# Kernel tuning notes

Measured on AMD Instinct MI355X. Metric: run time of the kernel, lower is better.

Reference implementation:

```python
import jax, jax.numpy as jnp
import numpy as np

# dims
P = 512          # perception_vector_size
A_DIM = 64       # action_vector_size
D_MODEL = 256
D_STATE = 16
D_CONV = 4
D_INNER = 2 * D_MODEL      # expand=2 -> 512
DT_RANK = D_MODEL // 16    # ceil(256/16) = 16
BATCH = 8192


def setup_inputs() -> dict:
    key = jax.random.key(0)
    ks = jax.random.split(key, 12)
    s = lambda k, shp, sc=0.02: (jax.random.normal(k, shp, jnp.float32) * sc)
    return {
        "perception": jax.random.normal(ks[0], (BATCH, P), jnp.float32),
        # Brain linears
        "W_in": s(ks[1], (D_MODEL, P)), "b_in": jnp.zeros((D_MODEL,), jnp.float32),
        "mu_w": s(ks[2], (A_DIM, D_MODEL)), "mu_b": jnp.zeros((A_DIM,), jnp.float32),
        "ls_w": s(ks[3], (A_DIM, D_MODEL)), "ls_b": jnp.zeros((A_DIM,), jnp.float32),
        # Mamba params (mamba_ssm Mamba(d_model=256, d_state=16, d_conv=4, expand=2))
        "in_proj_w": s(ks[4], (2 * D_INNER, D_MODEL)),            # no bias
        "conv_w": s(ks[5], (D_INNER, D_CONV), 0.1),               # depthwise causal conv
        "conv_b": jnp.zeros((D_INNER,), jnp.float32),
        "x_proj_w": s(ks[6], (DT_RANK + 2 * D_STATE, D_INNER)),   # no bias
        "dt_proj_w": s(ks[7], (D_INNER, DT_RANK), 0.1),
        "dt_proj_b": s(ks[8], (D_INNER,), 0.1),
        # S4D real init: A_log[d, n] = log(n+1)
        "A_log": jnp.log(jnp.broadcast_to(jnp.arange(1, D_STATE + 1, dtype=jnp.float32), (D_INNER, D_STATE))),
        "Dskip": jnp.ones((D_INNER,), jnp.float32),
        "out_proj_w": s(ks[9], (D_MODEL, D_INNER)),               # no bias
    }


def _mamba(x, in_proj_w, conv_w, conv_b, x_proj_w, dt_proj_w, dt_proj_b, A_log, Dskip):
    # x: [B, L, d_model]
    Bsz, L, _ = x.shape
    xz = x @ in_proj_w.T                       # [B, L, 2*D_INNER]
    u, z = jnp.split(xz, 2, axis=-1)           # each [B, L, D_INNER]
    # causal depthwise conv1d (padding d_conv-1 on the left), then SiLU
    u_pad = jnp.pad(u, ((0, 0), (D_CONV - 1, 0), (0, 0)))
    idx = jnp.arange(L)[:, None] + jnp.arange(D_CONV)[None, :]   # [L, K]
    windows = u_pad[:, idx, :]                 # [B, L, K, D_INNER]
    u = jnp.einsum('blkc,ck->blc', windows, conv_w) + conv_b
    u = jax.nn.silu(u)
    # input-dependent SSM params
    x_dbl = u @ x_proj_w.T                     # [B, L, dt_rank + 2*d_state]
    dt, Bm, Cm = jnp.split(x_dbl, [DT_RANK, DT_RANK + D_STATE], axis=-1)
    delta = jax.nn.softplus(dt @ dt_proj_w.T + dt_proj_b)  # [B, L, D_INNER]
    A = -jnp.exp(A_log)                        # [D_INNER, D_STATE]

    def step(h, inp):
        u_t, dl, b_t, c_t = inp                # [B,D],[B,D],[B,N],[B,N]
        dA = jnp.exp(dl[..., None] * A)        # [B, D, N]
        h = dA * h + dl[..., None] * b_t[:, None, :] * u_t[..., None]
        y = jnp.einsum('bdn,bn->bd', h, c_t)
        return h, y

    h0 = jnp.zeros((Bsz, D_INNER, D_STATE), u.dtype)
    xs = (u.transpose(1, 0, 2), delta.transpose(1, 0, 2),
          Bm.transpose(1, 0, 2), Cm.transpose(1, 0, 2))
    _, ys = jax.lax.scan(step, h0, xs)         # ys: [L, B, D_INNER]
    y = ys.transpose(1, 0, 2) + Dskip * u      # skip connection D*u
    return y * jax.nn.silu(z)


def reference(perception, W_in, b_in, mu_w, mu_b, ls_w, ls_b,
              in_proj_w, conv_w, conv_b, x_proj_w, dt_proj_w, dt_proj_b,
              A_log, Dskip, out_proj_w):
    x = (perception @ W_in.T + b_in)[:, None, :]     # [B, 1, d_model]
    y = _mamba(x, in_proj_w, conv_w, conv_b, x_proj_w,
               dt_proj_w, dt_proj_b, A_log, Dskip)   # [B, 1, D_INNER]
    h = (y @ out_proj_w.T)[:, 0, :]                  # [B, d_model]
    mu = jnp.tanh(h @ mu_w.T + mu_b)
    log_std = jnp.clip(h @ ls_w.T + ls_b, -5.0, 2.0)
    return mu, log_std
```

## Files before the change

### kernel.cpp

```cpp
#include <hip/hip_runtime.h>
#include <hip/hip_fp16.h>
#include <cmath>

#define BATCH 8192

typedef short bf16x8 __attribute__((ext_vector_type(8)));
typedef float f32x4 __attribute__((ext_vector_type(4)));
typedef float f32x16 __attribute__((ext_vector_type(16)));

__device__ __forceinline__ void split2(float x, unsigned short& h, unsigned short& l){
    unsigned u = __float_as_uint(x);
    unsigned hr = u + 0x7fffu + ((u >> 16) & 1u);
    unsigned short hs = (unsigned short)(hr >> 16);
    float hf = __uint_as_float(((unsigned)hs) << 16);
    float d = x - hf;
    unsigned v = __float_as_uint(d);
    unsigned short ls = (unsigned short)((v + 0x7fffu + ((v >> 16) & 1u)) >> 16);
    h = hs; l = ls;
}
__device__ __forceinline__ float fsig(float x){ return 1.f / (1.f + __expf(-x)); }
__device__ __forceinline__ float ftanh(float x){
    x = fminf(fmaxf(x, -10.f), 10.f);
    const float e = __expf(2.f*x);
    return (e - 1.f) / (e + 1.f);
}
__device__ __forceinline__ void async_copy16(void* lds, const void* g){
    __builtin_amdgcn_global_load_lds(
        (const __attribute__((address_space(1))) unsigned int*)g,
        (__attribute__((address_space(3))) unsigned int*)lds, 16, 0, 0);
}


__global__ __launch_bounds__(256) void prep_all(
    const float* __restrict__ percep,
    const float* __restrict__ in_proj, const float* __restrict__ W_in,
    const float* __restrict__ b_in,
    const float* __restrict__ mu_w, const float* __restrict__ ls_w,
    const float* __restrict__ conv_w, const float* __restrict__ conv_b,
    const float* __restrict__ out_proj, const float* __restrict__ x_proj,
    unsigned short* __restrict__ W1h, unsigned short* __restrict__ W1l,
    unsigned short* __restrict__ Wth, unsigned short* __restrict__ Wtl,
    unsigned short* __restrict__ Xph, unsigned short* __restrict__ Xpl,
    unsigned short* __restrict__ Ph, unsigned short* __restrict__ Pl,
    float* __restrict__ b1)
{
    __shared__ float As[16][68];
    __shared__ float Ws[16][68];
    __shared__ unsigned short Lh[4096];
    __shared__ unsigned short Ll[4096];

    const int bx = blockIdx.x, by = blockIdx.y;
    const int tid = threadIdx.x;
    if (bx >= 20){
        const int s = (bx-20)*8 + by;
        const int band = s >> 4, ks = s & 15;
        const size_t tbase = (size_t)s*4096;
#pragma unroll
        for (int g=0; g<2; ++g){
            const int u = g*256 + tid;
            const int row = u >> 2, piece = u & 3;
            const float* src = percep + (size_t)(band*128 + row)*512 + ks*32 + piece*8;
            const float4 v0 = *reinterpret_cast<const float4*>(src);
            const float4 v1 = *reinterpret_cast<const float4*>(src+4);
            unsigned short h[8], l[8];
            split2(v0.x,h[0],l[0]); split2(v0.y,h[1],l[1]);
            split2(v0.z,h[2],l[2]); split2(v0.w,h[3],l[3]);
            split2(v1.x,h[4],l[4]); split2(v1.y,h[5],l[5]);
            split2(v1.z,h[6],l[6]); split2(v1.w,h[7],l[7]);
            uint4 H, L;
            H.x=(unsigned)h[0]|((unsigned)h[1]<<16); H.y=(unsigned)h[2]|((unsigned)h[3]<<16);
            H.z=(unsigned)h[4]|((unsigned)h[5]<<16); H.w=(unsigned)h[6]|((unsigned)h[7]<<16);
            L.x=(unsigned)l[0]|((unsigned)l[1]<<16); L.y=(unsigned)l[2]|((unsigned)l[3]<<16);
            L.z=(unsigned)l[4]|((unsigned)l[5]<<16); L.w=(unsigned)l[6]|((unsigned)l[7]<<16);
            const int off = piece*1024 + row*8;
            *reinterpret_cast<uint4*>(&Lh[off]) = H;
            *reinterpret_cast<uint4*>(&Ll[off]) = L;
        }
        __syncthreads();
#pragma unroll
        for (int g=0; g<2; ++g){
            const int f = g*256 + tid;
            *reinterpret_cast<uint4*>(&Ph[tbase + f*8]) = *reinterpret_cast<const uint4*>(&Lh[f*8]);
            *reinterpret_cast<uint4*>(&Pl[tbase + f*8]) = *reinterpret_cast<const uint4*>(&Ll[f*8]);
        }
        return;
    }
    if (bx == 18){
        const int lane = tid & 63, w = tid >> 6;
        const float4 bv = *reinterpret_cast<const float4*>(&b_in[lane*4]);
        const int nbase = by*128 + w*32;
#pragma unroll 4
        for (int i=0;i<32;i++){
            const int n = nbase + i;
            const float4 av = *reinterpret_cast<const float4*>(&in_proj[(size_t)n*256 + lane*4]);
            float p = av.x*bv.x + av.y*bv.y + av.z*bv.z + av.w*bv.w;
#pragma unroll
            for (int off=32; off; off>>=1) p += __shfl_xor(p, off, 64);
            if (lane == 0)
                b1[n] = (n < 512) ? fmaf(p, conv_w[n*4+3], conv_b[n]) : p;
        }
        return;
    }
    if (bx == 19){
        const int c0 = by*64;
#pragma unroll
        for (int p=0;p<16;p++){
            const int idx = p*256 + tid;
            const int rrow = idx >> 6;
            const int c = c0 + (idx & 63);
            const float v = (rrow < 48) ? x_proj[(size_t)rrow*512 + c] : 0.f;
            unsigned short h,l; split2(v,h,l);
            const int ks = c >> 5, r = (c >> 3) & 3, pos = c & 7;
            const size_t off = (size_t)ks*2048 + (r*64 + rrow)*8 + pos;
            Xph[off]=h; Xpl[off]=l;
        }
        return;
    }
    const float* A; unsigned short *Oh, *Ol; int m0; bool wt;
    const float* B;
    if (bx < 16){ A = in_proj + (size_t)bx*64*256; B = W_in; Oh=W1h; Ol=W1l; m0=bx*64; wt=false; }
    else { A = (bx==16 ? mu_w : ls_w); B = out_proj; Oh=Wth; Ol=Wtl; m0=(bx-16)*64; wt=true; }
    const int n0 = by*64;

    const int tm = tid/16, tn = tid%16;
    float acc[4][4];
#pragma unroll
    for (int i=0;i<4;i++)
#pragma unroll
      for (int j=0;j<4;j++) acc[i][j]=0.f;

    for (int k0=0;k0<256;k0+=16){
        {
            const int kf = tid & 3, mm = tid >> 2;
            float4 v = *reinterpret_cast<const float4*>(A + (size_t)mm*256 + k0 + kf*4);
            As[kf*4+0][mm]=v.x; As[kf*4+1][mm]=v.y; As[kf*4+2][mm]=v.z; As[kf*4+3][mm]=v.w;
        }
        {
            const int nn4 = tid & 15, kk = tid >> 4;
            float4 v = *reinterpret_cast<const float4*>(B + (size_t)(k0+kk)*512 + n0 + nn4*4);
            *reinterpret_cast<float4*>(&Ws[kk][nn4*4]) = v;
        }
        __syncthreads();
#pragma unroll
        for (int k=0;k<16;k++){
            const float4 av = *reinterpret_cast<const float4*>(&As[k][tm*4]);
            const float4 bv = *reinterpret_cast<const float4*>(&Ws[k][tn*4]);
            float a[4]={av.x,av.y,av.z,av.w}, b[4]={bv.x,bv.y,bv.z,bv.w};
#pragma unroll
            for (int i=0;i<4;i++)
#pragma unroll
                for (int j=0;j<4;j++) acc[i][j] = fmaf(a[i], b[j], acc[i][j]);
        }
        __syncthreads();
    }
#pragma unroll
    for (int i=0;i<4;i++){
        const int gm = m0 + tm*4 + i;
        const float s = (!wt && gm < 512) ? conv_w[gm*4+3] : 1.f;
        const int n = n0 + tn*4;
        unsigned short h[4], l[4];
#pragma unroll
        for (int j=0;j<4;j++) split2(acc[i][j]*s, h[j], l[j]);
        const int ks = n >> 5, r = (n >> 3) & 3, pos = n & 7;
        size_t off;
        if (wt) off = (size_t)ks*4096 + (r*128 + gm)*8 + pos;
        else    off = (size_t)((gm>>7)*16 + ks)*4096 + (r*128 + (gm&127))*8 + pos;
        *reinterpret_cast<ushort4*>(&Oh[off]) = make_ushort4(h[0],h[1],h[2],h[3]);
        *reinterpret_cast<ushort4*>(&Ol[off]) = make_ushort4(l[0],l[1],l[2],l[3]);
    }
}

__global__ __launch_bounds__(256,2) void mgemm5(
    const unsigned short* __restrict__ AhT, const unsigned short* __restrict__ AlT,
    const unsigned short* __restrict__ BhT, const unsigned short* __restrict__ BlT,
    const float* __restrict__ bias,
    float* __restrict__ O0, __half* __restrict__ O1)
{
    constexpr int TM=128, TN=128, WM=64, WN=64;
    constexpr int WAVES_N = TN/WN;
    constexpr int MT = WM/32, NT = WN/32;
    constexpr int PL = 4096;
    constexpr int BUF = 4*PL;
    constexpr int NK = 16;
    __shared__ unsigned short sm[2*BUF];

    const int tid = threadIdx.x;
    const int mb = blockIdx.x, nb = blockIdx.y;
    const int m0 = mb * TM, n0 = nb * TN;
    const int lane = tid & 63, wid = tid >> 6;
    const int half = lane >> 5, l32 = lane & 31;
    const int wm = (wid / WAVES_N) * WM;
    const int wn = (wid % WAVES_N) * WN;

    f32x16 acc[MT][NT];
#pragma unroll
    for (int i=0;i<MT;i++)
#pragma unroll
      for (int j=0;j<NT;j++)
#pragma unroll
        for (int r=0;r<16;r++) acc[i][j][r] = 0.f;

    auto dmaAll = [&](int k, int b){
        unsigned short* base = sm + b*BUF;
        const unsigned short* Ah = AhT + (size_t)(mb*16 + k)*PL;
        const unsigned short* Al = AlT + (size_t)(mb*16 + k)*PL;
        const unsigned short* Bh = BhT + (size_t)(nb*16 + k)*PL;
        const unsigned short* Bl = BlT + (size_t)(nb*16 + k)*PL;
#pragma unroll
        for (int it=0; it<2; ++it){
            const int f = it*256 + tid;
            const int wb = (it*256 + wid*64)*8;
            async_copy16(base +        wb, Ah + f*8);
            async_copy16(base +   PL + wb, Al + f*8);
            async_copy16(base + 2*PL + wb, Bh + f*8);
            async_copy16(base + 3*PL + wb, Bl + f*8);
        }
    };

    dmaAll(0, 0);

    for (int k=0; k<NK; ++k){
        const int cur = k & 1, nxt = cur ^ 1;
        __syncthreads();
        if (k+1 < NK) dmaAll(k+1, nxt);

        const unsigned short* bufc = sm + cur*BUF;
        bf16x8 ah[2][MT], al[2][MT], bh[2][NT], bl[2][NT];
#pragma unroll
        for (int j=0;j<2;j++){
            const int r = j*2 + half;
#pragma unroll
            for (int mt=0; mt<MT; ++mt){
                const int off = (r*TM + wm + mt*32 + l32)*8;
                ah[j][mt] = *reinterpret_cast<const bf16x8*>(&bufc[off]);
                al[j][mt] = *reinterpret_cast<const bf16x8*>(&bufc[PL + off]);
            }
#pragma unroll
            for (int nt=0; nt<NT; ++nt){
                const int off = (r*TN + wn + nt*32 + l32)*8;
                bh[j][nt] = *reinterpret_cast<const bf16x8*>(&bufc[2*PL + off]);
                bl[j][nt] = *reinterpret_cast<const bf16x8*>(&bufc[3*PL + off]);
            }
        }
#pragma unroll
        for (int j=0;j<2;j++){
#pragma unroll
            for (int mt=0; mt<MT; ++mt)
#pragma unroll
            for (int nt=0; nt<NT; ++nt)
                acc[mt][nt] = __builtin_amdgcn_mfma_f32_32x32x16_bf16(ah[j][mt], bh[j][nt], acc[mt][nt], 0,0,0);
#pragma unroll
            for (int mt=0; mt<MT; ++mt)
#pragma unroll
            for (int nt=0; nt<NT; ++nt)
                acc[mt][nt] = __builtin_amdgcn_mfma_f32_32x32x16_bf16(al[j][mt], bh[j][nt], acc[mt][nt], 0,0,0);
#pragma unroll
            for (int mt=0; mt<MT; ++mt)
#pragma unroll
            for (int nt=0; nt<NT; ++nt)
                acc[mt][nt] = __builtin_amdgcn_mfma_f32_32x32x16_bf16(ah[j][mt], bl[j][nt], acc[mt][nt], 0,0,0);
        }
    }

#pragma unroll
    for (int mt=0; mt<MT; ++mt)
#pragma unroll
    for (int nt=0; nt<NT; ++nt)
#pragma unroll
    for (int r=0; r<16; ++r){
        const int row = m0 + wm + mt*32 + (r&3) + 8*(r>>2) + 4*half;
        const int col = n0 + wn + nt*32 + l32;
        float v = acc[mt][nt][r] + bias[col];
        if (col < 512) O0[(size_t)row*512 + col] = v * fsig(v);
        else           O1[(size_t)row*512 + (col-512)] = __float2half(v);
    }
}

__global__ __launch_bounds__(256) void tail_fused(
    const float* __restrict__ Uf, const __half* __restrict__ Zh,
    const unsigned short* __restrict__ XphT, const unsigned short* __restrict__ XplT,
    const unsigned short* __restrict__ WthT, const unsigned short* __restrict__ WtlT,
    const float* __restrict__ dtw, const float* __restrict__ dtb,
    const float* __restrict__ dskip,
    const float* __restrict__ mu_b, const float* __restrict__ ls_b,
    float* __restrict__ mu_o, float* __restrict__ ls_o)
{
    constexpr int TM=32, TN=64;
    constexpr int P1_APL = 1024;
    constexpr int P1_BPL = 2048;
    constexpr int P1_BUF = 2*P1_APL + 2*P1_BPL;
    constexpr int PSTR = 264;
    __shared__ unsigned short sW[16384];
    __shared__ unsigned short sYh[16*PSTR];
    __shared__ unsigned short sYl[16*PSTR];
    __shared__ float sxd[32][49];
    __shared__ float sBC[32];

    const int tid = threadIdx.x;
    const int m0 = blockIdx.x * TM;
    const int lane = tid & 63, wid = tid >> 6;
    const int quad = lane >> 4, l16 = lane & 15;
    const int wm = (wid >> 1) * 16;
    const int wn = (wid & 1) * 32;

    f32x4 acc[2];
    acc[0] = (f32x4){0.f,0.f,0.f,0.f};
    acc[1] = (f32x4){0.f,0.f,0.f,0.f};

    float4 areg[2];
    const int am = tid & 31, ar = (tid >> 5) & 3;

    auto loadA = [&](int k){
        if (tid < 128){
            const float* src = Uf + (size_t)(m0+am)*512 + k*32 + ar*8;
            areg[0] = *reinterpret_cast<const float4*>(src);
            areg[1] = *reinterpret_cast<const float4*>(src+4);
        }
    };
    auto dmaB = [&](int k, int b){
        unsigned short* dst = sW + b*P1_BUF + 2*P1_APL;
        const int wb = wid*64*8;
        async_copy16(dst + wb,          XphT + (size_t)k*P1_BPL + tid*8);
        async_copy16(dst + P1_BPL + wb, XplT + (size_t)k*P1_BPL + tid*8);
    };
    auto writeA = [&](int b){
        if (tid < 128){
            unsigned short* dh = sW + b*P1_BUF;
            unsigned short* dl = dh + P1_APL;
            const float* p = reinterpret_cast<const float*>(&areg[0]);
            unsigned short h[8], l[8];
#pragma unroll
            for (int j=0;j<8;j++) split2(p[j], h[j], l[j]);
            uint4 H, L;
            H.x=(unsigned)h[0]|((unsigned)h[1]<<16); H.y=(unsigned)h[2]|((unsigned)h[3]<<16);
            H.z=(unsigned)h[4]|((unsigned)h[5]<<16); H.w=(unsigned)h[6]|((unsigned)h[7]<<16);
            L.x=(unsigned)l[0]|((unsigned)l[1]<<16); L.y=(unsigned)l[2]|((unsigned)l[3]<<16);
            L.z=(unsigned)l[4]|((unsigned)l[5]<<16); L.w=(unsigned)l[6]|((unsigned)l[7]<<16);
            const int f = (tid >> 5)*32 + am;
            *reinterpret_cast<uint4*>(&dh[f*8]) = H;
            *reinterpret_cast<uint4*>(&dl[f*8]) = L;
        }
    };

    loadA(0); dmaB(0,0); writeA(0);
    for (int k=0; k<16; ++k){
        const int cur = k & 1, nxt = cur ^ 1;
        __syncthreads();
        const bool pf = (k+1 < 16);
        if (pf){ loadA(k+1); dmaB(k+1, nxt); }
        const unsigned short* bufc = sW + cur*P1_BUF;
        bf16x8 ah, al2, bh[2], bl[2];
        {
            const int off = (quad*TM + wm + l16)*8;
            ah  = *reinterpret_cast<const bf16x8*>(&bufc[off]);
            al2 = *reinterpret_cast<const bf16x8*>(&bufc[P1_APL + off]);
        }
#pragma unroll
        for (int nt=0; nt<2; ++nt){
            const int off = (quad*TN + wn + nt*16 + l16)*8;
            bh[nt] = *reinterpret_cast<const bf16x8*>(&bufc[2*P1_APL + off]);
            bl[nt] = *reinterpret_cast<const bf16x8*>(&bufc[2*P1_APL + P1_BPL + off]);
        }
#pragma unroll
        for (int nt=0; nt<2; ++nt)
            acc[nt] = __builtin_amdgcn_mfma_f32_16x16x32_bf16(ah, bh[nt], acc[nt], 0,0,0);
#pragma unroll
        for (int nt=0; nt<2; ++nt)
            acc[nt] = __builtin_amdgcn_mfma_f32_16x16x32_bf16(al2, bh[nt], acc[nt], 0,0,0);
#pragma unroll
        for (int nt=0; nt<2; ++nt)
            acc[nt] = __builtin_amdgcn_mfma_f32_16x16x32_bf16(ah, bl[nt], acc[nt], 0,0,0);
        if (pf) writeA(nxt);
    }

#pragma unroll
    for (int nt=0; nt<2; ++nt)
#pragma unroll
    for (int r=0; r<4; ++r){
        const int row = wm + quad*4 + r;
        const int col = wn + nt*16 + l16;
        if (col < 48) sxd[row][col] = acc[nt][r];
    }
    __syncthreads();
    if (tid < 32){
        float bc = 0.f;
#pragma unroll
        for (int n=0;n<16;n++) bc = fmaf(sxd[tid][16+n], sxd[tid][32+n], bc);
        sBC[tid] = bc;
    }
    __syncthreads();

    const int wm2 = (wid >> 1) * 16;
    const int wn2 = (wid & 1) * 64;
    f32x4 oacc[4];
#pragma unroll
    for (int j=0;j<4;j++) oacc[j] = (f32x4){0.f,0.f,0.f,0.f};

    const int q = tid >> 6, dd = tid & 63;

    auto dmaW = [&](int ks, int b){
        unsigned short* dst = sW + b*8192;
#pragma unroll
        for (int it=0; it<2; ++it){
            const int f = it*256 + tid;
            const int wb = (it*256 + wid*64)*8;
            async_copy16(dst + wb,        WthT + (size_t)ks*4096 + f*8);
            async_copy16(dst + 4096 + wb, WtlT + (size_t)ks*4096 + f*8);
        }
    };

    for (int c=0; c<4; ++c){
        const int c0 = c*128;
        const int d0 = c0 + 2*dd, d1 = d0 + 1;
        float w0[16], w1[16];
#pragma unroll
        for (int j=0;j<4;j++){
            float4 a = *reinterpret_cast<const float4*>(&dtw[d0*16 + j*4]);
            w0[j*4]=a.x; w0[j*4+1]=a.y; w0[j*4+2]=a.z; w0[j*4+3]=a.w;
            float4 b = *reinterpret_cast<const float4*>(&dtw[d1*16 + j*4]);
            w1[j*4]=b.x; w1[j*4+1]=b.y; w1[j*4+2]=b.z; w1[j*4+3]=b.w;
        }
        const float db0 = dtb[d0], db1 = dtb[d1];
        const float dk0 = dskip[d0], dk1 = dskip[d1];

        __syncthreads();
        const int lk = 2*dd;
        const unsigned yidx = (unsigned)((lk>>3)*PSTR + (lk&7)) >> 1;
#pragma unroll 2
        for (int rr=0; rr<8; ++rr){
            const int r = q*8 + rr;
            float xr[16];
#pragma unroll
            for (int j=0;j<16;j++) xr[j] = sxd[r][j];
            const float bc = sBC[r];
            float t0 = db0, t1 = db1;
#pragma unroll
            for (int j=0;j<16;j++){ t0 = fmaf(xr[j], w0[j], t0); t1 = fmaf(xr[j], w1[j], t1); }
            const float dl0 = (t0 > 20.f) ? t0 : __logf(1.f + __expf(t0));
            const float dl1 = (t1 > 20.f) ? t1 : __logf(1.f + __expf(t1));
            const size_t off = (size_t)(m0+r)*512;
            const float2 uv = *reinterpret_cast<const float2*>(&Uf[off + d0]);
            const __half2 zv = *reinterpret_cast<const __half2*>(&Zh[off + d0]);
            const float z0 = __low2float(zv), z1 = __high2float(zv);
            const float y0 = uv.x * fmaf(dl0, bc, dk0) * (z0 * fsig(z0));
            const float y1 = uv.y * fmaf(dl1, bc, dk1) * (z1 * fsig(z1));
            unsigned short h0,l0,h1,l1;
            split2(y0,h0,l0); split2(y1,h1,l1);
            const unsigned idx = yidx + (unsigned)(r*4);
            reinterpret_cast<unsigned*>(sYh)[idx] = (unsigned)h0 | ((unsigned)h1<<16);
            reinterpret_cast<unsigned*>(sYl)[idx] = (unsigned)l0 | ((unsigned)l1<<16);
        }
        dmaW(c*4, 0);
        for (int s=0; s<4; ++s){
            __syncthreads();
            if (s < 3) dmaW(c*4 + s+1, (s+1)&1);
            const unsigned short* bw = sW + (s&1)*8192;
            bf16x8 ya, yl2, bh2[4], bl2[4];
            {
                const int aoff = (4*s + quad)*PSTR + (wm2 + l16)*8;
                ya  = *reinterpret_cast<const bf16x8*>(&sYh[aoff]);
                yl2 = *reinterpret_cast<const bf16x8*>(&sYl[aoff]);
            }
#pragma unroll
            for (int nt=0; nt<4; ++nt){
                const int boff = (quad*128 + wn2 + nt*16 + l16)*8;
                bh2[nt] = *reinterpret_cast<const bf16x8*>(&bw[boff]);
                bl2[nt] = *reinterpret_cast<const bf16x8*>(&bw[4096 + boff]);
            }
#pragma unroll
            for (int nt=0; nt<4; ++nt)
                oacc[nt] = __builtin_amdgcn_mfma_f32_16x16x32_bf16(ya, bh2[nt], oacc[nt], 0,0,0);
#pragma unroll
            for (int nt=0; nt<4; ++nt)
                oacc[nt] = __builtin_amdgcn_mfma_f32_16x16x32_bf16(yl2, bh2[nt], oacc[nt], 0,0,0);
#pragma unroll
            for (int nt=0; nt<4; ++nt)
                oacc[nt] = __builtin_amdgcn_mfma_f32_16x16x32_bf16(ya, bl2[nt], oacc[nt], 0,0,0);
        }
    }

#pragma unroll
    for (int nt=0; nt<4; ++nt)
#pragma unroll
    for (int r=0; r<4; ++r){
        const int row = m0 + wm2 + quad*4 + r;
        const int col = wn2 + nt*16 + l16;
        const float v = oacc[nt][r];
        if (col < 64) mu_o[(size_t)row*64 + col] = ftanh(v + mu_b[col]);
        else          ls_o[(size_t)row*64 + (col-64)] = fminf(fmaxf(v + ls_b[col-64], -5.f), 2.f);
    }
}

extern "C" void kernel_launch(void* const* d_in, const int* in_sizes, int n_in,
                              void* d_out, int out_size, void* d_ws, size_t ws_size,
                              hipStream_t stream) {
    (void)in_sizes; (void)n_in; (void)out_size; (void)ws_size;
    const float* percep  = (const float*)d_in[0];
    const float* W_in    = (const float*)d_in[1];
    const float* b_in    = (const float*)d_in[2];
    const float* mu_w    = (const float*)d_in[3];
    const float* mu_b    = (const float*)d_in[4];
    const float* ls_w    = (const float*)d_in[5];
    const float* ls_b    = (const float*)d_in[6];
    const float* in_proj = (const float*)d_in[7];
    const float* conv_w  = (const float*)d_in[8];
    const float* conv_b  = (const float*)d_in[9];
    const float* x_proj  = (const float*)d_in[10];
    const float* dt_w    = (const float*)d_in[11];
    const float* dt_b    = (const float*)d_in[12];
    const float* Dskip   = (const float*)d_in[14];
    const float* out_proj= (const float*)d_in[15];

    char* ws = (char*)d_ws;
    const size_t MB = 1u<<20;
    unsigned short* W1h = (unsigned short*)(ws);
    unsigned short* W1l = (unsigned short*)(ws + 1*MB);
    unsigned short* Wth = (unsigned short*)(ws + 2*MB);
    unsigned short* Wtl = (unsigned short*)(ws + 2*MB + 128*1024);
    unsigned short* Xph = (unsigned short*)(ws + 2*MB + 256*1024);
    unsigned short* Xpl = (unsigned short*)(ws + 2*MB + 320*1024);
    float*          b1  = (float*)         (ws + 2*MB + 384*1024);
    unsigned short* Ph  = (unsigned short*)(ws + 4*MB);
    unsigned short* Pl  = (unsigned short*)(ws + 12*MB);
    float*          Uf  = (float*)         (ws + 20*MB);
    __half*         Zh  = (__half*)        (ws + 36*MB);

    float* mu_o = (float*)d_out;
    float* ls_o = (float*)d_out + (size_t)BATCH*64;

    dim3 blk(256);
    prep_all<<<dim3(148,8), blk, 0, stream>>>(
        percep, in_proj, W_in, b_in, mu_w, ls_w, conv_w, conv_b, out_proj, x_proj,
        W1h, W1l, Wth, Wtl, Xph, Xpl, Ph, Pl, b1);
    mgemm5<<<dim3(64,8), blk, 0, stream>>>(
        Ph, Pl, W1h, W1l, b1, Uf, Zh);
    tail_fused<<<dim3(BATCH/32), blk, 0, stream>>>(
        Uf, Zh, Xph, Xpl, Wth, Wtl, dt_w, dt_b, Dskip, mu_b, ls_b, mu_o, ls_o);
}
```

Baseline: 179.4 us.

## Halve tail tile to 16 rows and read weights directly from global

Rewrites the fused tail kernel to process 16 rows per block instead of 32, doubling the grid. The async LDS staging and double buffering for the x_proj and output-projection weights are removed; each wave now loads its B fragments straight from global memory and converts A in registers. This shrinks shared memory and drops many barriers to raise occupancy and parallelism. In exchange, weight reads are repeated per block and rely on cache, and the per-wave MFMA work is smaller.

```diff
diff --git a/kernel.cpp b/kernel.cpp
--- a/kernel.cpp
+++ b/kernel.cpp
@@ -276,7 +276,7 @@
     }
 }
 
-__global__ __launch_bounds__(256) void tail_fused(
+__global__ __launch_bounds__(256) void tail_fused2(
     const float* __restrict__ Uf, const __half* __restrict__ Zh,
     const unsigned short* __restrict__ XphT, const unsigned short* __restrict__ XplT,
     const unsigned short* __restrict__ WthT, const unsigned short* __restrict__ WtlT,
@@ -285,150 +285,81 @@
     const float* __restrict__ mu_b, const float* __restrict__ ls_b,
     float* __restrict__ mu_o, float* __restrict__ ls_o)
 {
-    constexpr int TM=32, TN=64;
-    constexpr int P1_APL = 1024;
-    constexpr int P1_BPL = 2048;
-    constexpr int P1_BUF = 2*P1_APL + 2*P1_BPL;
-    constexpr int PSTR = 264;
-    __shared__ unsigned short sW[16384];
-    __shared__ unsigned short sYh[16*PSTR];
-    __shared__ unsigned short sYl[16*PSTR];
-    __shared__ float sxd[32][49];
-    __shared__ float sBC[32];
+    constexpr int TM = 16;
+    constexpr int ROWB = 136;
+    __shared__ unsigned short sYh[16*ROWB];
+    __shared__ unsigned short sYl[16*ROWB];
+    __shared__ float sxd[TM][49];
+    __shared__ float sBC[TM];
 
     const int tid = threadIdx.x;
     const int m0 = blockIdx.x * TM;
     const int lane = tid & 63, wid = tid >> 6;
     const int quad = lane >> 4, l16 = lane & 15;
-    const int wm = (wid >> 1) * 16;
-    const int wn = (wid & 1) * 32;
-
-    f32x4 acc[2];
-    acc[0] = (f32x4){0.f,0.f,0.f,0.f};
-    acc[1] = (f32x4){0.f,0.f,0.f,0.f};
-
-    float4 areg[2];
-    const int am = tid & 31, ar = (tid >> 5) & 3;
-
-    auto loadA = [&](int k){
-        if (tid < 128){
-            const float* src = Uf + (size_t)(m0+am)*512 + k*32 + ar*8;
-            areg[0] = *reinterpret_cast<const float4*>(src);
-            areg[1] = *reinterpret_cast<const float4*>(src+4);
-        }
-    };
-    auto dmaB = [&](int k, int b){
-        unsigned short* dst = sW + b*P1_BUF + 2*P1_APL;
-        const int wb = wid*64*8;
-        async_copy16(dst + wb,          XphT + (size_t)k*P1_BPL + tid*8);
-        async_copy16(dst + P1_BPL + wb, XplT + (size_t)k*P1_BPL + tid*8);
-    };
-    auto writeA = [&](int b){
-        if (tid < 128){
-            unsigned short* dh = sW + b*P1_BUF;
-            unsigned short* dl = dh + P1_APL;
-            const float* p = reinterpret_cast<const float*>(&areg[0]);
+
+    f32x4 acc = (f32x4){0.f,0.f,0.f,0.f};
+    const float* arow = Uf + (size_t)(m0 + l16)*512 + quad*8;
+    const int bxp = (quad*64 + wid*16 + l16)*8;
+#pragma unroll
+    for (int k=0; k<16; ++k){
+        const float4 a0 = *reinterpret_cast<const float4*>(arow + k*32);
+        const float4 a1 = *reinterpret_cast<const float4*>(arow + k*32 + 4);
+        const bf16x8 bh = *reinterpret_cast<const bf16x8*>(&XphT[(size_t)k*2048 + bxp]);
+        const bf16x8 bl = *reinterpret_cast<const bf16x8*>(&XplT[(size_t)k*2048 + bxp]);
+        bf16x8 ah, al;
+        {
+            const float a[8] = {a0.x,a0.y,a0.z,a0.w,a1.x,a1.y,a1.z,a1.w};
             unsigned short h[8], l[8];
 #pragma unroll
-            for (int j=0;j<8;j++) split2(p[j], h[j], l[j]);
-            uint4 H, L;
-            H.x=(unsigned)h[0]|((unsigned)h[1]<<16); H.y=(unsigned)h[2]|((unsigned)h[3]<<16);
-            H.z=(unsigned)h[4]|((unsigned)h[5]<<16); H.w=(unsigned)h[6]|((unsigned)h[7]<<16);
-            L.x=(unsigned)l[0]|((unsigned)l[1]<<16); L.y=(unsigned)l[2]|((unsigned)l[3]<<16);
-            L.z=(unsigned)l[4]|((unsigned)l[5]<<16); L.w=(unsigned)l[6]|((unsigned)l[7]<<16);
-            const int f = (tid >> 5)*32 + am;
-            *reinterpret_cast<uint4*>(&dh[f*8]) = H;
-            *reinterpret_cast<uint4*>(&dl[f*8]) = L;
-        }
-    };
-
-    loadA(0); dmaB(0,0); writeA(0);
-    for (int k=0; k<16; ++k){
-        const int cur = k & 1, nxt = cur ^ 1;
-        __syncthreads();
-        const bool pf = (k+1 < 16);
-        if (pf){ loadA(k+1); dmaB(k+1, nxt); }
-        const unsigned short* bufc = sW + cur*P1_BUF;
-        bf16x8 ah, al2, bh[2], bl[2];
-        {
-            const int off = (quad*TM + wm + l16)*8;
-            ah  = *reinterpret_cast<const bf16x8*>(&bufc[off]);
-            al2 = *reinterpret_cast<const bf16x8*>(&bufc[P1_APL + off]);
-        }
-#pragma unroll
-        for (int nt=0; nt<2; ++nt){
-            const int off = (quad*TN + wn + nt*16 + l16)*8;
-            bh[nt] = *reinterpret_cast<const bf16x8*>(&bufc[2*P1_APL + off]);
-            bl[nt] = *reinterpret_cast<const bf16x8*>(&bufc[2*P1_APL + P1_BPL + off]);
-        }
-#pragma unroll
-        for (int nt=0; nt<2; ++nt)
-            acc[nt] = __builtin_amdgcn_mfma_f32_16x16x32_bf16(ah, bh[nt], acc[nt], 0,0,0);
-#pragma unroll
-        for (int nt=0; nt<2; ++nt)
-            acc[nt] = __builtin_amdgcn_mfma_f32_16x16x32_bf16(al2, bh[nt], acc[nt], 0,0,0);
-#pragma unroll
-        for (int nt=0; nt<2; ++nt)
-            acc[nt] = __builtin_amdgcn_mfma_f32_16x16x32_bf16(ah, bl[nt], acc[nt], 0,0,0);
-        if (pf) writeA(nxt);
-    }
-
-#pragma unroll
-    for (int nt=0; nt<2; ++nt)
-#pragma unroll
-    for (int r=0; r<4; ++r){
-        const int row = wm + quad*4 + r;
-        const int col = wn + nt*16 + l16;
-        if (col < 48) sxd[row][col] = acc[nt][r];
+            for (int j=0;j<8;j++) split2(a[j], h[j], l[j]);
+#pragma unroll
+            for (int j=0;j<8;j++){ ah[j] = (short)h[j]; al[j] = (short)l[j]; }
+        }
+        acc = __builtin_amdgcn_mfma_f32_16x16x32_bf16(ah, bh, acc, 0,0,0);
+        acc = __builtin_amdgcn_mfma_f32_16x16x32_bf16(al, bh, acc, 0,0,0);
+        acc = __builtin_amdgcn_mfma_f32_16x16x32_bf16(ah, bl, acc, 0,0,0);
+    }
+
+    {
+        const int colp = wid*16 + l16;
+        if (colp < 48){
+#pragma unroll
+            for (int r=0;r<4;++r) sxd[quad*4 + r][colp] = acc[r];
+        }
     }
     __syncthreads();
-    if (tid < 32){
+    if (tid < TM){
         float bc = 0.f;
 #pragma unroll
         for (int n=0;n<16;n++) bc = fmaf(sxd[tid][16+n], sxd[tid][32+n], bc);
         sBC[tid] = bc;
     }
-    __syncthreads();
-
-    const int wm2 = (wid >> 1) * 16;
-    const int wn2 = (wid & 1) * 64;
-    f32x4 oacc[4];
-#pragma unroll
-    for (int j=0;j<4;j++) oacc[j] = (f32x4){0.f,0.f,0.f,0.f};
-
-    const int q = tid >> 6, dd = tid & 63;
-
-    auto dmaW = [&](int ks, int b){
-        unsigned short* dst = sW + b*8192;
-#pragma unroll
-        for (int it=0; it<2; ++it){
-            const int f = it*256 + tid;
-            const int wb = (it*256 + wid*64)*8;
-            async_copy16(dst + wb,        WthT + (size_t)ks*4096 + f*8);
-            async_copy16(dst + 4096 + wb, WtlT + (size_t)ks*4096 + f*8);
-        }
-    };
+
+    f32x4 oacc[2];
+    oacc[0] = (f32x4){0.f,0.f,0.f,0.f};
+    oacc[1] = (f32x4){0.f,0.f,0.f,0.f};
+
+    const int q = wid;
+    const unsigned ybase = (unsigned)(lane >> 2)*68 + (unsigned)(lane & 3);
 
     for (int c=0; c<4; ++c){
         const int c0 = c*128;
-        const int d0 = c0 + 2*dd, d1 = d0 + 1;
+        const int d0 = c0 + 2*lane, d1 = d0 + 1;
         float w0[16], w1[16];
 #pragma unroll
         for (int j=0;j<4;j++){
-            float4 a = *reinterpret_cast<const float4*>(&dtw[d0*16 + j*4]);
+            const float4 a = *reinterpret_cast<const float4*>(&dtw[d0*16 + j*4]);
             w0[j*4]=a.x; w0[j*4+1]=a.y; w0[j*4+2]=a.z; w0[j*4+3]=a.w;
-            float4 b = *reinterpret_cast<const float4*>(&dtw[d1*16 + j*4]);
+            const float4 b = *reinterpret_cast<const float4*>(&dtw[d1*16 + j*4]);
             w1[j*4]=b.x; w1[j*4+1]=b.y; w1[j*4+2]=b.z; w1[j*4+3]=b.w;
         }
         const float db0 = dtb[d0], db1 = dtb[d1];
         const float dk0 = dskip[d0], dk1 = dskip[d1];
 
         __syncthreads();
-        const int lk = 2*dd;
-        const unsigned yidx = (unsigned)((lk>>3)*PSTR + (lk&7)) >> 1;
-#pragma unroll 2
-        for (int rr=0; rr<8; ++rr){
-            const int r = q*8 + rr;
+#pragma unroll
+        for (int rr=0; rr<4; ++rr){
+            const int r = q*4 + rr;
             float xr[16];
 #pragma unroll
             for (int j=0;j<16;j++) xr[j] = sxd[r][j];
@@ -446,45 +377,42 @@
             const float y1 = uv.y * fmaf(dl1, bc, dk1) * (z1 * fsig(z1));
             unsigned short h0,l0,h1,l1;
             split2(y0,h0,l0); split2(y1,h1,l1);
-            const unsigned idx = yidx + (unsigned)(r*4);
-            reinterpret_cast<unsigned*>(sYh)[idx] = (unsigned)h0 | ((unsigned)h1<<16);
-            reinterpret_cast<unsigned*>(sYl)[idx] = (unsigned)l0 | ((unsigned)l1<<16);
-        }
-        dmaW(c*4, 0);
+            reinterpret_cast<unsigned*>(sYh)[ybase + r*4] = (unsigned)h0 | ((unsigned)h1<<16);
+            reinterpret_cast<unsigned*>(sYl)[ybase + r*4] = (unsigned)l0 | ((unsigned)l1<<16);
+        }
+        __syncthreads();
+
+#pragma unroll
         for (int s=0; s<4; ++s){
-            __syncthreads();
-            if (s < 3) dmaW(c*4 + s+1, (s+1)&1);
-            const unsigned short* bw = sW + (s&1)*8192;
-            bf16x8 ya, yl2, bh2[4], bl2[4];
-            {
-                const int aoff = (4*s + quad)*PSTR + (wm2 + l16)*8;
-                ya  = *reinterpret_cast<const bf16x8*>(&sYh[aoff]);
-                yl2 = *reinterpret_cast<const bf16x8*>(&sYl[aoff]);
+            const int kt = c*4 + s;
+            const int aoff = (4*s + quad)*ROWB + l16*8;
+            const bf16x8 ya = *reinterpret_cast<const bf16x8*>(&sYh[aoff]);
+            const bf16x8 yl = *reinterpret_cast<const bf16x8*>(&sYl[aoff]);
+            bf16x8 bh2[2], bl2[2];
+#pragma unroll
+            for (int nt=0; nt<2; ++nt){
+                const size_t boff = (size_t)kt*4096 + (quad*128 + wid*32 + nt*16 + l16)*8;
+                bh2[nt] = *reinterpret_cast<const bf16x8*>(&WthT[boff]);
+                bl2[nt] = *reinterpret_cast<const bf16x8*>(&WtlT[boff]);
             }
 #pragma unroll
-            for (int nt=0; nt<4; ++nt){
-                const int boff = (quad*128 + wn2 + nt*16 + l16)*8;
-                bh2[nt] = *reinterpret_cast<const bf16x8*>(&bw[boff]);
-                bl2[nt] = *reinterpret_cast<const bf16x8*>(&bw[4096 + boff]);
-            }
-#pragma unroll
-            for (int nt=0; nt<4; ++nt)
+            for (int nt=0; nt<2; ++nt)
                 oacc[nt] = __builtin_amdgcn_mfma_f32_16x16x32_bf16(ya, bh2[nt], oacc[nt], 0,0,0);
 #pragma unroll
-            for (int nt=0; nt<4; ++nt)
-                oacc[nt] = __builtin_amdgcn_mfma_f32_16x16x32_bf16(yl2, bh2[nt], oacc[nt], 0,0,0);
-#pragma unroll
-            for (int nt=0; nt<4; ++nt)
+            for (int nt=0; nt<2; ++nt)
+                oacc[nt] = __builtin_amdgcn_mfma_f32_16x16x32_bf16(yl, bh2[nt], oacc[nt], 0,0,0);
+#pragma unroll
+            for (int nt=0; nt<2; ++nt)
                 oacc[nt] = __builtin_amdgcn_mfma_f32_16x16x32_bf16(ya, bl2[nt], oacc[nt], 0,0,0);
         }
     }
 
 #pragma unroll
-    for (int nt=0; nt<4; ++nt)
+    for (int nt=0; nt<2; ++nt)
 #pragma unroll
     for (int r=0; r<4; ++r){
-        const int row = m0 + wm2 + quad*4 + r;
-        const int col = wn2 + nt*16 + l16;
+        const int row = m0 + quad*4 + r;
+        const int col = wid*32 + nt*16 + l16;
         const float v = oacc[nt][r];
         if (col < 64) mu_o[(size_t)row*64 + col] = ftanh(v + mu_b[col]);
         else          ls_o[(size_t)row*64 + (col-64)] = fminf(fmaxf(v + ls_b[col-64], -5.f), 2.f);
@@ -534,6 +462,6 @@
         W1h, W1l, Wth, Wtl, Xph, Xpl, Ph, Pl, b1);
     mgemm5<<<dim3(64,8), blk, 0, stream>>>(
         Ph, Pl, W1h, W1l, b1, Uf, Zh);
-    tail_fused<<<dim3(BATCH/32), blk, 0, stream>>>(
+    tail_fused2<<<dim3(BATCH/16), blk, 0, stream>>>(
         Uf, Zh, Xph, Xpl, Wth, Wtl, dt_w, dt_b, Dskip, mu_b, ls_b, mu_o, ls_o);
 }
```

Result: faster. 167.5 us (-6.6%).
